# Kernel tuning notes

Measured on AMD Instinct MI355X. Metric: run time of the kernel, lower is better.

## Reference

```python
import jax, jax.numpy as jnp
import numpy as np

HEADS = 16
EMBED = 1024
HEAD_DIM = EMBED // HEADS


def setup_inputs() -> dict:
    key = jax.random.key(0)
    ks = jax.random.split(key, 10)
    B, SQ, SKV = 2, 2048, 2048
    s = 1.0 / np.sqrt(HEAD_DIM)
    sd = 1.0 / np.sqrt(EMBED)
    return {
        "queries": jax.random.normal(ks[0], (B, SQ, EMBED), jnp.float32),
        "values": jax.random.normal(ks[1], (B, SKV, EMBED), jnp.float32),
        "heads": HEADS,
        "Wv": jax.random.normal(ks[2], (HEAD_DIM, HEAD_DIM), jnp.float32) * s,
        "bv": jax.random.normal(ks[3], (HEAD_DIM,), jnp.float32) * 0.02,
        "Wk": jax.random.normal(ks[4], (HEAD_DIM, HEAD_DIM), jnp.float32) * s,
        "bk": jax.random.normal(ks[5], (HEAD_DIM,), jnp.float32) * 0.02,
        "Wq": jax.random.normal(ks[6], (HEAD_DIM, HEAD_DIM), jnp.float32) * s,
        "bq": jax.random.normal(ks[7], (HEAD_DIM,), jnp.float32) * 0.02,
        "Wd": jax.random.normal(ks[8], (EMBED, EMBED), jnp.float32) * sd,
        "bd": jax.random.normal(ks[9], (EMBED,), jnp.float32) * 0.02,
    }


def reference(queries, values, heads, Wv, bv, Wk, bk, Wq, bq, Wd, bd):
    n, sq, e = queries.shape
    skv = values.shape[1]
    d = e // heads
    # reshape to per-head layout [b, s, h, d]
    q_in = queries.reshape(n, sq, heads, d)
    v_in = values.reshape(n, skv, heads, d)
    # shared per-head linear projections (torch Linear: x @ W.T + b)
    v = jnp.einsum("bshd,ed->bshe", v_in, Wv) + bv
    # quirk preserved: keys computed from the ALREADY-PROJECTED values
    k = jnp.einsum("bshd,ed->bshe", v, Wk) + bk
    q = jnp.einsum("bshd,ed->bshe", q_in, Wq) + bq
    # full O(n^2) score matrix [b, h, sq, skv] (as in source)
    scores = jnp.einsum("bqhd,bkhd->bhqk", q, k) / jnp.sqrt(jnp.asarray(d, q.dtype))
    attn = jax.nn.softmax(scores, axis=-1)
    out = jnp.einsum("bhqk,bkhd->bqhd", attn, v).reshape(n, sq, e)
    return out @ Wd.T + bd
```

## Files before the change

kernel.cpp:

```cpp
#include <hip/hip_runtime.h>
#include <hip/hip_bf16.h>
#include <hip/hip_fp16.h>
#include <math.h>

typedef _Float16 f16;
typedef _Float16 f16x8 __attribute__((ext_vector_type(8)));
typedef _Float16 f16x4 __attribute__((ext_vector_type(4)));
typedef _Float16 f16x2 __attribute__((ext_vector_type(2)));
typedef unsigned short u16x8v __attribute__((ext_vector_type(8)));
typedef float f32x4 __attribute__((ext_vector_type(4)));

namespace {
constexpr int B = 2;
constexpr int H = 16;
constexpr int S = 2048;
constexpr int D = 64;
constexpr int E = 1024;
constexpr int LP = 72;
constexpr float QSCALE = 0.125f * 1.4426950408889634f;
}

#define GLOBAL_LOAD_LDS16(gp, lp)                                              \
  __builtin_amdgcn_global_load_lds(                                            \
      (const __attribute__((address_space(1))) void*)(gp),                     \
      (__attribute__((address_space(3))) void*)(lp), 16, 0, 0)

__global__ __launch_bounds__(256) void prep(const float* __restrict__ Wd, f16* __restrict__ wd16,
                                            const float* __restrict__ Wk, const float* __restrict__ Wv,
                                            const float* __restrict__ bv, const float* __restrict__ bk,
                                            float* __restrict__ Wkv, float* __restrict__ bkv) {
  if (blockIdx.x < 1024) {
    const int i = blockIdx.x * 256 + threadIdx.x;
    const float4 f = ((const float4*)Wd)[i];
    f16x4 o;
    o.x = (f16)f.x; o.y = (f16)f.y; o.z = (f16)f.z; o.w = (f16)f.w;
    *(f16x4*)(wd16 + 4 * (size_t)i) = o;
  } else {
    const int g = (blockIdx.x - 1024) * 256 + threadIdx.x;
    const int i = g >> 6, j = g & 63;
    float s = 0.f;
#pragma unroll 16
    for (int d = 0; d < 64; ++d) s = fmaf(Wk[i * 64 + d], Wv[d * 64 + j], s);
    Wkv[g] = s;
    if (g < 64) {
      float bb = bk[g];
#pragma unroll 16
      for (int d = 0; d < 64; ++d) bb = fmaf(Wk[g * 64 + d], bv[d], bb);
      bkv[g] = bb;
    }
  }
}

__global__ __launch_bounds__(256) void proj3_mfma(const float* __restrict__ xq,
                                                  const float* __restrict__ xv,
                                                  const float* __restrict__ Wq,
                                                  const float* __restrict__ bq,
                                                  const float* __restrict__ Wv,
                                                  const float* __restrict__ bv,
                                                  const float* __restrict__ Wkv,
                                                  const float* __restrict__ bkv,
                                                  f16* __restrict__ qp,
                                                  f16* __restrict__ vp,
                                                  f16* __restrict__ kp) {
  const int which = blockIdx.y;
  const float* x    = (which == 0) ? xq : xv;
  const float* W    = (which == 0) ? Wq : (which == 1) ? Wv : Wkv;
  const float* bias = (which == 0) ? bq : (which == 1) ? bv : bkv;
  f16* out          = (which == 0) ? qp : (which == 1) ? vp : kp;
  const float scale = (which == 0) ? QSCALE : 1.0f;

  const int t = threadIdx.x, lane = t & 63, w = t >> 6;
  const int l15 = lane & 15, quad = lane >> 4;
  const int m0 = (blockIdx.x * 4 + w) * 64;

  f16x8 wf[4][2], af[4][2];
#pragma unroll
  for (int nt = 0; nt < 4; ++nt)
#pragma unroll
    for (int kc = 0; kc < 2; ++kc) {
      const float* g = W + (size_t)(nt * 16 + l15) * 64 + kc * 32 + quad * 8;
      const float4 a = *(const float4*)g, b2 = *(const float4*)(g + 4);
      f16x8 v;
      v[0]=(f16)a.x; v[1]=(f16)a.y; v[2]=(f16)a.z; v[3]=(f16)a.w;
      v[4]=(f16)b2.x; v[5]=(f16)b2.y; v[6]=(f16)b2.z; v[7]=(f16)b2.w;
      wf[nt][kc] = v;
    }
#pragma unroll
  for (int mt = 0; mt < 4; ++mt)
#pragma unroll
    for (int kc = 0; kc < 2; ++kc) {
      const float* g = x + (size_t)(m0 + mt * 16 + l15) * 64 + kc * 32 + quad * 8;
      const float4 a = *(const float4*)g, b2 = *(const float4*)(g + 4);
      f16x8 v;
      v[0]=(f16)a.x; v[1]=(f16)a.y; v[2]=(f16)a.z; v[3]=(f16)a.w;
      v[4]=(f16)b2.x; v[5]=(f16)b2.y; v[6]=(f16)b2.z; v[7]=(f16)b2.w;
      af[mt][kc] = v;
    }

  f32x4 acc[4][4];
#pragma unroll
  for (int nt = 0; nt < 4; ++nt)
#pragma unroll
    for (int mt = 0; mt < 4; ++mt) acc[nt][mt] = (f32x4){0.f, 0.f, 0.f, 0.f};
#pragma unroll
  for (int kc = 0; kc < 2; ++kc)
#pragma unroll
    for (int nt = 0; nt < 4; ++nt)
#pragma unroll
      for (int mt = 0; mt < 4; ++mt)
        acc[nt][mt] = __builtin_amdgcn_mfma_f32_16x16x32_f16(wf[nt][kc], af[mt][kc], acc[nt][mt], 0, 0, 0);

  float4 bl4[4];
#pragma unroll
  for (int nt = 0; nt < 4; ++nt) bl4[nt] = *(const float4*)&bias[nt * 16 + quad * 4];

#pragma unroll
  for (int mt = 0; mt < 4; ++mt) {
    const int g = m0 + mt * 16 + l15;
    const int h = g & 15, bs_ = g >> 4;
    const int b = bs_ >> 11, s = bs_ & 2047;
    f16* o = out + ((size_t)(b * H + h) * S + s) * 64 + quad * 4;
#pragma unroll
    for (int nt = 0; nt < 4; ++nt) {
      const float p0 = (acc[nt][mt][0] + bl4[nt].x) * scale;
      const float p1 = (acc[nt][mt][1] + bl4[nt].y) * scale;
      const float p2 = (acc[nt][mt][2] + bl4[nt].z) * scale;
      const float p3 = (acc[nt][mt][3] + bl4[nt].w) * scale;
      union { f16x4 v4; f16x2 hh[2]; } u;
      u.hh[0] = __builtin_bit_cast(f16x2, __builtin_amdgcn_cvt_pkrtz(p0, p1));
      u.hh[1] = __builtin_bit_cast(f16x2, __builtin_amdgcn_cvt_pkrtz(p2, p3));
      *(f16x4*)(o + nt * 16) = u.v4;
    }
  }
}

__global__ __launch_bounds__(256) void attn_mfma(const f16* __restrict__ qp,
                                                 const f16* __restrict__ kp,
                                                 const f16* __restrict__ vp,
                                                 f16* __restrict__ ao) {
  __shared__ f16 ks[2][64 * LP];
  __shared__ f16 vt[2][64 * LP];
  __shared__ f16 ps[4 * 32 * LP];
  const int t = threadIdx.x, lane = t & 63, w = t >> 6;
  const int l15 = lane & 15, quad = lane >> 4;
  const int bh = blockIdx.x;
  const int q0 = blockIdx.y * 128;
  const f16* qbase = qp + ((size_t)bh * S + q0 + w * 32) * D;
  const f16* kbase = kp + (size_t)bh * S * D;
  const f16* vbase = vp + (size_t)bh * S * D;
  f16* pw = ps + w * 32 * LP;

  const int kr = t >> 2, kc0 = (t & 3) * 16;
  const int vd0 = (t >> 5) * 8, vpc0 = (t & 31) * 2;
  const int vkva = (vpc0 & 3) * 16 + (vpc0 >> 2);

  f16x8 qf[2][2];
#pragma unroll
  for (int mt = 0; mt < 2; ++mt)
#pragma unroll
    for (int kc = 0; kc < 2; ++kc)
      qf[mt][kc] = *(const f16x8*)(qbase + (size_t)(mt * 16 + l15) * D + kc * 32 + quad * 8);

  f16x8 vb4;
#pragma unroll
  for (int j = 0; j < 8; ++j) vb4[j] = (l15 == 0) ? (f16)1.0f : (f16)0.0f;

  f32x4 O[2][5];
#pragma unroll
  for (int mt = 0; mt < 2; ++mt)
#pragma unroll
    for (int nt = 0; nt < 5; ++nt) O[mt][nt] = (f32x4){0.f, 0.f, 0.f, 0.f};

  u16x8v ka, kb2, va, vb2;
  {
    const f16* gk = kbase + (size_t)kr * D + kc0;
    ka  = *(const u16x8v*)gk;
    kb2 = *(const u16x8v*)(gk + 8);
    const f16* gv = vbase + (size_t)vkva * D + vd0;
    va  = *(const u16x8v*)gv;
    vb2 = *(const u16x8v*)(gv + 16 * D);
  }
  {
    *(u16x8v*)&ks[0][kr * LP + kc0]     = ka;
    *(u16x8v*)&ks[0][kr * LP + kc0 + 8] = kb2;
#pragma unroll
    for (int j = 0; j < 8; ++j) {
      const unsigned pk = (unsigned)va[j] | ((unsigned)vb2[j] << 16);
      *(unsigned*)&vt[0][(vd0 + j) * LP + vpc0] = pk;
    }
  }

  int cur = 0;
  for (int kt = 0; kt < S / 64; ++kt) {
    if (kt + 1 < S / 64) {
      const f16* gk = kbase + ((size_t)(kt + 1) * 64 + kr) * D + kc0;
      ka  = *(const u16x8v*)gk;
      kb2 = *(const u16x8v*)(gk + 8);
      const f16* gv = vbase + ((size_t)(kt + 1) * 64 + vkva) * D + vd0;
      va  = *(const u16x8v*)gv;
      vb2 = *(const u16x8v*)(gv + 16 * D);
    }
    __asm__ volatile("s_waitcnt lgkmcnt(0)" ::: "memory");
    __builtin_amdgcn_s_barrier();
    __asm__ volatile("" ::: "memory");

    f32x4 sc[2][4];
#pragma unroll
    for (int mt = 0; mt < 2; ++mt)
#pragma unroll
      for (int nt = 0; nt < 4; ++nt) sc[mt][nt] = (f32x4){0.f, 0.f, 0.f, 0.f};
    __builtin_amdgcn_s_setprio(1);
#pragma unroll
    for (int kc = 0; kc < 2; ++kc)
#pragma unroll
      for (int nt = 0; nt < 4; ++nt) {
        const f16x8 bf = *(const f16x8*)&ks[cur][(nt * 16 + l15) * LP + kc * 32 + quad * 8];
#pragma unroll
        for (int mt = 0; mt < 2; ++mt)
          sc[mt][nt] = __builtin_amdgcn_mfma_f32_16x16x32_f16(qf[mt][kc], bf, sc[mt][nt], 0, 0, 0);
      }
    __builtin_amdgcn_s_setprio(0);

#pragma unroll
    for (int mt = 0; mt < 2; ++mt)
#pragma unroll
      for (int r = 0; r < 4; ++r) {
        const float p0 = __builtin_amdgcn_exp2f(sc[mt][0][r]);
        const float p1 = __builtin_amdgcn_exp2f(sc[mt][1][r]);
        const float p2 = __builtin_amdgcn_exp2f(sc[mt][2][r]);
        const float p3 = __builtin_amdgcn_exp2f(sc[mt][3][r]);
        union { f16x4 v4; f16x2 h[2]; } u;
        u.h[0] = __builtin_bit_cast(f16x2, __builtin_amdgcn_cvt_pkrtz(p0, p1));
        u.h[1] = __builtin_bit_cast(f16x2, __builtin_amdgcn_cvt_pkrtz(p2, p3));
        *(f16x4*)&pw[(mt * 16 + quad * 4 + r) * LP + l15 * 4] = u.v4;
      }
    __asm__ volatile("s_waitcnt lgkmcnt(0)" ::: "memory");

    f16x8 pa[2][2];
#pragma unroll
    for (int mt = 0; mt < 2; ++mt)
#pragma unroll
      for (int kc = 0; kc < 2; ++kc)
        pa[mt][kc] = *(const f16x8*)&pw[(mt * 16 + l15) * LP + kc * 32 + quad * 8];
    __builtin_amdgcn_s_setprio(1);
#pragma unroll
    for (int kc = 0; kc < 2; ++kc) {
#pragma unroll
      for (int nt = 0; nt < 4; ++nt) {
        const f16x8 vbf = *(const f16x8*)&vt[cur][(nt * 16 + l15) * LP + kc * 32 + quad * 8];
#pragma unroll
        for (int mt = 0; mt < 2; ++mt)
          O[mt][nt] = __builtin_amdgcn_mfma_f32_16x16x32_f16(pa[mt][kc], vbf, O[mt][nt], 0, 0, 0);
      }
#pragma unroll
      for (int mt = 0; mt < 2; ++mt)
        O[mt][4] = __builtin_amdgcn_mfma_f32_16x16x32_f16(pa[mt][kc], vb4, O[mt][4], 0, 0, 0);
    }
    __builtin_amdgcn_s_setprio(0);

    if (kt + 1 < S / 64) {
      const int nb = cur ^ 1;
      *(u16x8v*)&ks[nb][kr * LP + kc0]     = ka;
      *(u16x8v*)&ks[nb][kr * LP + kc0 + 8] = kb2;
#pragma unroll
      for (int j = 0; j < 8; ++j) {
        const unsigned pk = (unsigned)va[j] | ((unsigned)vb2[j] << 16);
        *(unsigned*)&vt[nb][(vd0 + j) * LP + vpc0] = pk;
      }
    }
    cur ^= 1;
  }

  const int b = bh >> 4, h = bh & 15;
#pragma unroll
  for (int mt = 0; mt < 2; ++mt)
#pragma unroll
    for (int r = 0; r < 4; ++r) {
      const float l = __shfl(O[mt][4][r], quad << 4, 64);
      const float inv = 1.f / l;
      const int row = q0 + w * 32 + mt * 16 + quad * 4 + r;
      f16* o = ao + ((size_t)b * S + row) * E + h * D;
#pragma unroll
      for (int nt = 0; nt < 4; ++nt)
        o[nt * 16 + l15] = (f16)(O[mt][nt][r] * inv);
    }
}

__global__ __launch_bounds__(256) void dense_mfma(const f16* __restrict__ A,
                                                  const f16* __restrict__ Wd16,
                                                  const float* __restrict__ bd,
                                                  float* __restrict__ out) {
  __shared__ f16 as[2][128 * 64];
  __shared__ f16 bs[2][128 * 64];
  const int t = threadIdx.x;
  const int lane = t & 63;
  const int w = t >> 6;
  const int l15 = lane & 15;
  const int quad = lane >> 4;
  const int m0 = blockIdx.x * 128;
  const int n0 = blockIdx.y * 128;
  const int wm = (w >> 1) * 64, wn = (w & 1) * 64;

  const int srow = (lane >> 3);
  const int scol = (lane & 7) * 8;
  const f16* ga0 = A    + (size_t)(m0 + w * 32 + srow) * E + scol;
  const f16* gb0 = Wd16 + (size_t)(n0 + w * 32 + srow) * E + scol;

  constexpr int NT = E / 64;

  f32x4 acc[4][4];
#pragma unroll
  for (int mt = 0; mt < 4; ++mt)
#pragma unroll
    for (int nt = 0; nt < 4; ++nt) acc[mt][nt] = (f32x4){0.f, 0.f, 0.f, 0.f};

#pragma unroll
  for (int i = 0; i < 4; ++i) {
    GLOBAL_LOAD_LDS16(ga0 + (size_t)(i * 8) * E, &as[0][(w * 32 + i * 8) * 64]);
    GLOBAL_LOAD_LDS16(gb0 + (size_t)(i * 8) * E, &bs[0][(w * 32 + i * 8) * 64]);
  }
  __syncthreads();

  int cur = 0;
  for (int kt = 0; kt < NT; ++kt) {
    if (kt + 1 < NT) {
      const int nb = cur ^ 1;
#pragma unroll
      for (int i = 0; i < 4; ++i) {
        GLOBAL_LOAD_LDS16(ga0 + (size_t)(i * 8) * E + (kt + 1) * 64, &as[nb][(w * 32 + i * 8) * 64]);
        GLOBAL_LOAD_LDS16(gb0 + (size_t)(i * 8) * E + (kt + 1) * 64, &bs[nb][(w * 32 + i * 8) * 64]);
      }
    }
    f16x8 af[4][2];
#pragma unroll
    for (int mt = 0; mt < 4; ++mt)
#pragma unroll
      for (int kc = 0; kc < 2; ++kc)
        af[mt][kc] = *(const f16x8*)&as[cur][(wm + mt * 16 + l15) * 64 + kc * 32 + quad * 8];
#pragma unroll
    for (int kc = 0; kc < 2; ++kc)
#pragma unroll
      for (int nt = 0; nt < 4; ++nt) {
        const f16x8 bf = *(const f16x8*)&bs[cur][(wn + nt * 16 + l15) * 64 + kc * 32 + quad * 8];
#pragma unroll
        for (int mt = 0; mt < 4; ++mt)
          acc[mt][nt] = __builtin_amdgcn_mfma_f32_16x16x32_f16(af[mt][kc], bf, acc[mt][nt], 0, 0, 0);
      }
    __syncthreads();
    cur ^= 1;
  }

#pragma unroll
  for (int nt = 0; nt < 4; ++nt) {
    const int col = n0 + wn + nt * 16 + l15;
    const float bdv = bd[col];
#pragma unroll
    for (int mt = 0; mt < 4; ++mt)
#pragma unroll
      for (int r = 0; r < 4; ++r)
        out[(size_t)(m0 + wm + mt * 16 + quad * 4 + r) * E + col] = acc[mt][nt][r] + bdv;
  }
}

extern "C" void kernel_launch(void* const* d_in, const int* in_sizes, int n_in,
                              void* d_out, int out_size, void* d_ws, size_t ws_size,
                              hipStream_t stream) {
  const float* queries = (const float*)d_in[0];
  const float* values  = (const float*)d_in[1];
  const float* Wv = (const float*)d_in[3];
  const float* bv = (const float*)d_in[4];
  const float* Wk = (const float*)d_in[5];
  const float* bk = (const float*)d_in[6];
  const float* Wq = (const float*)d_in[7];
  const float* bq = (const float*)d_in[8];
  const float* Wd = (const float*)d_in[9];
  const float* bd = (const float*)d_in[10];
  float* out = (float*)d_out;

  char* ws = (char*)d_ws;
  f16* qp    = (f16*)(ws);
  f16* kp    = (f16*)(ws + 8u * 1024 * 1024);
  f16* vp    = (f16*)(ws + 16u * 1024 * 1024);
  f16* ao    = (f16*)(ws + 24u * 1024 * 1024);
  f16* wd16  = (f16*)(ws + 32u * 1024 * 1024);
  float* wkv = (float*)(ws + 34u * 1024 * 1024);
  float* bkv = (float*)(ws + 34u * 1024 * 1024 + 16384);
  (void)ws_size; (void)in_sizes; (void)n_in; (void)out_size;

  prep<<<1040, 256, 0, stream>>>(Wd, wd16, Wk, Wv, bv, bk, wkv, bkv);
  proj3_mfma<<<dim3(256, 3), 256, 0, stream>>>(queries, values, Wq, bq, Wv, bv, wkv, bkv, qp, vp, kp);
  attn_mfma<<<dim3(B * H, S / 128), 256, 0, stream>>>(qp, kp, vp, ao);
  dense_mfma<<<dim3(B * S / 128, E / 128), 256, 0, stream>>>(ao, wd16, bd, out);
}
```

Measured before the change: 187.9 us.

## Swizzle LDS tiles, keep P in registers, and share values load across projections

```diff
diff --git a/kernel.cpp b/kernel.cpp
--- a/kernel.cpp
+++ b/kernel.cpp
@@ -16,7 +16,6 @@
 constexpr int S = 2048;
 constexpr int D = 64;
 constexpr int E = 1024;
-constexpr int LP = 72;
 constexpr float QSCALE = 0.125f * 1.4426950408889634f;
 }
 
@@ -63,28 +62,13 @@
                                                   f16* __restrict__ vp,
                                                   f16* __restrict__ kp) {
   const int which = blockIdx.y;
-  const float* x    = (which == 0) ? xq : xv;
-  const float* W    = (which == 0) ? Wq : (which == 1) ? Wv : Wkv;
-  const float* bias = (which == 0) ? bq : (which == 1) ? bv : bkv;
-  f16* out          = (which == 0) ? qp : (which == 1) ? vp : kp;
-  const float scale = (which == 0) ? QSCALE : 1.0f;
+  const float* x = which ? xv : xq;
 
   const int t = threadIdx.x, lane = t & 63, w = t >> 6;
   const int l15 = lane & 15, quad = lane >> 4;
   const int m0 = (blockIdx.x * 4 + w) * 64;
 
-  f16x8 wf[4][2], af[4][2];
-#pragma unroll
-  for (int nt = 0; nt < 4; ++nt)
-#pragma unroll
-    for (int kc = 0; kc < 2; ++kc) {
-      const float* g = W + (size_t)(nt * 16 + l15) * 64 + kc * 32 + quad * 8;
-      const float4 a = *(const float4*)g, b2 = *(const float4*)(g + 4);
-      f16x8 v;
-      v[0]=(f16)a.x; v[1]=(f16)a.y; v[2]=(f16)a.z; v[3]=(f16)a.w;
-      v[4]=(f16)b2.x; v[5]=(f16)b2.y; v[6]=(f16)b2.z; v[7]=(f16)b2.w;
-      wf[nt][kc] = v;
-    }
+  f16x8 af[4][2];
 #pragma unroll
   for (int mt = 0; mt < 4; ++mt)
 #pragma unroll
@@ -97,39 +81,60 @@
       af[mt][kc] = v;
     }
 
-  f32x4 acc[4][4];
-#pragma unroll
-  for (int nt = 0; nt < 4; ++nt)
-#pragma unroll
-    for (int mt = 0; mt < 4; ++mt) acc[nt][mt] = (f32x4){0.f, 0.f, 0.f, 0.f};
-#pragma unroll
-  for (int kc = 0; kc < 2; ++kc)
+  const int npass = which ? 2 : 1;
+  for (int pass = 0; pass < npass; ++pass) {
+    const float* W    = which ? (pass ? Wkv : Wv) : Wq;
+    const float* bias = which ? (pass ? bkv : bv) : bq;
+    f16* out          = which ? (pass ? kp : vp) : qp;
+    const float scale = which ? 1.0f : QSCALE;
+
+    f16x8 wf[4][2];
 #pragma unroll
     for (int nt = 0; nt < 4; ++nt)
 #pragma unroll
-      for (int mt = 0; mt < 4; ++mt)
-        acc[nt][mt] = __builtin_amdgcn_mfma_f32_16x16x32_f16(wf[nt][kc], af[mt][kc], acc[nt][mt], 0, 0, 0);
-
-  float4 bl4[4];
-#pragma unroll
-  for (int nt = 0; nt < 4; ++nt) bl4[nt] = *(const float4*)&bias[nt * 16 + quad * 4];
-
-#pragma unroll
-  for (int mt = 0; mt < 4; ++mt) {
-    const int g = m0 + mt * 16 + l15;
-    const int h = g & 15, bs_ = g >> 4;
-    const int b = bs_ >> 11, s = bs_ & 2047;
-    f16* o = out + ((size_t)(b * H + h) * S + s) * 64 + quad * 4;
-#pragma unroll
-    for (int nt = 0; nt < 4; ++nt) {
-      const float p0 = (acc[nt][mt][0] + bl4[nt].x) * scale;
-      const float p1 = (acc[nt][mt][1] + bl4[nt].y) * scale;
-      const float p2 = (acc[nt][mt][2] + bl4[nt].z) * scale;
-      const float p3 = (acc[nt][mt][3] + bl4[nt].w) * scale;
-      union { f16x4 v4; f16x2 hh[2]; } u;
-      u.hh[0] = __builtin_bit_cast(f16x2, __builtin_amdgcn_cvt_pkrtz(p0, p1));
-      u.hh[1] = __builtin_bit_cast(f16x2, __builtin_amdgcn_cvt_pkrtz(p2, p3));
-      *(f16x4*)(o + nt * 16) = u.v4;
+      for (int kc = 0; kc < 2; ++kc) {
+        const float* g = W + (size_t)(nt * 16 + l15) * 64 + kc * 32 + quad * 8;
+        const float4 a = *(const float4*)g, b2 = *(const float4*)(g + 4);
+        f16x8 v;
+        v[0]=(f16)a.x; v[1]=(f16)a.y; v[2]=(f16)a.z; v[3]=(f16)a.w;
+        v[4]=(f16)b2.x; v[5]=(f16)b2.y; v[6]=(f16)b2.z; v[7]=(f16)b2.w;
+        wf[nt][kc] = v;
+      }
+
+    f32x4 acc[4][4];
+#pragma unroll
+    for (int nt = 0; nt < 4; ++nt)
+#pragma unroll
+      for (int mt = 0; mt < 4; ++mt) acc[nt][mt] = (f32x4){0.f, 0.f, 0.f, 0.f};
+#pragma unroll
+    for (int kc = 0; kc < 2; ++kc)
+#pragma unroll
+      for (int nt = 0; nt < 4; ++nt)
+#pragma unroll
+        for (int mt = 0; mt < 4; ++mt)
+          acc[nt][mt] = __builtin_amdgcn_mfma_f32_16x16x32_f16(wf[nt][kc], af[mt][kc], acc[nt][mt], 0, 0, 0);
+
+    float4 bl4[4];
+#pragma unroll
+    for (int nt = 0; nt < 4; ++nt) bl4[nt] = *(const float4*)&bias[nt * 16 + quad * 4];
+
+#pragma unroll
+    for (int mt = 0; mt < 4; ++mt) {
+      const int g = m0 + mt * 16 + l15;
+      const int h = g & 15, bs_ = g >> 4;
+      const int b = bs_ >> 11, s = bs_ & 2047;
+      f16* o = out + ((size_t)(b * H + h) * S + s) * 64 + quad * 4;
+#pragma unroll
+      for (int nt = 0; nt < 4; ++nt) {
+        const float p0 = (acc[nt][mt][0] + bl4[nt].x) * scale;
+        const float p1 = (acc[nt][mt][1] + bl4[nt].y) * scale;
+        const float p2 = (acc[nt][mt][2] + bl4[nt].z) * scale;
+        const float p3 = (acc[nt][mt][3] + bl4[nt].w) * scale;
+        union { f16x4 v4; f16x2 hh[2]; } u;
+        u.hh[0] = __builtin_bit_cast(f16x2, __builtin_amdgcn_cvt_pkrtz(p0, p1));
+        u.hh[1] = __builtin_bit_cast(f16x2, __builtin_amdgcn_cvt_pkrtz(p2, p3));
+        *(f16x4*)(o + nt * 16) = u.v4;
+      }
     }
   }
 }
@@ -138,9 +143,8 @@
                                                  const f16* __restrict__ kp,
                                                  const f16* __restrict__ vp,
                                                  f16* __restrict__ ao) {
-  __shared__ f16 ks[2][64 * LP];
-  __shared__ f16 vt[2][64 * LP];
-  __shared__ f16 ps[4 * 32 * LP];
+  __shared__ f16 ks[2][64 * 64];
+  __shared__ f16 vt[2][64 * 64];
   const int t = threadIdx.x, lane = t & 63, w = t >> 6;
   const int l15 = lane & 15, quad = lane >> 4;
   const int bh = blockIdx.x;
@@ -148,11 +152,12 @@
   const f16* qbase = qp + ((size_t)bh * S + q0 + w * 32) * D;
   const f16* kbase = kp + (size_t)bh * S * D;
   const f16* vbase = vp + (size_t)bh * S * D;
-  f16* pw = ps + w * 32 * LP;
-
-  const int kr = t >> 2, kc0 = (t & 3) * 16;
-  const int vd0 = (t >> 5) * 8, vpc0 = (t & 31) * 2;
-  const int vkva = (vpc0 & 3) * 16 + (vpc0 >> 2);
+
+  const int kr = t >> 2, kc2 = (t & 3) * 2;
+  const int vd0 = (t >> 5) * 8;
+  const int p0 = (t & 31) * 2;
+  const int vkv = ((p0 >> 5) << 5) | (((p0 & 7) >> 2) << 4) | (((p0 >> 3) & 3) << 2) | (p0 & 3);
+  const int vchunk = p0 >> 3, vsub = p0 & 7;
 
   f16x8 qf[2][2];
 #pragma unroll
@@ -173,81 +178,79 @@
 
   u16x8v ka, kb2, va, vb2;
   {
-    const f16* gk = kbase + (size_t)kr * D + kc0;
+    const f16* gk = kbase + (size_t)kr * D + kc2 * 8;
     ka  = *(const u16x8v*)gk;
     kb2 = *(const u16x8v*)(gk + 8);
-    const f16* gv = vbase + (size_t)vkva * D + vd0;
+    const f16* gv = vbase + (size_t)vkv * D + vd0;
     va  = *(const u16x8v*)gv;
-    vb2 = *(const u16x8v*)(gv + 16 * D);
+    vb2 = *(const u16x8v*)(gv + D);
   }
   {
-    *(u16x8v*)&ks[0][kr * LP + kc0]     = ka;
-    *(u16x8v*)&ks[0][kr * LP + kc0 + 8] = kb2;
+    *(u16x8v*)&ks[0][kr * 64 + ((kc2 ^ (kr & 7)) * 8)]       = ka;
+    *(u16x8v*)&ks[0][kr * 64 + (((kc2 + 1) ^ (kr & 7)) * 8)] = kb2;
 #pragma unroll
     for (int j = 0; j < 8; ++j) {
+      const int d = vd0 + j;
       const unsigned pk = (unsigned)va[j] | ((unsigned)vb2[j] << 16);
-      *(unsigned*)&vt[0][(vd0 + j) * LP + vpc0] = pk;
+      *(unsigned*)&vt[0][d * 64 + ((vchunk ^ (d & 7)) * 8) + vsub] = pk;
     }
   }
 
   int cur = 0;
   for (int kt = 0; kt < S / 64; ++kt) {
     if (kt + 1 < S / 64) {
-      const f16* gk = kbase + ((size_t)(kt + 1) * 64 + kr) * D + kc0;
+      const f16* gk = kbase + ((size_t)(kt + 1) * 64 + kr) * D + kc2 * 8;
       ka  = *(const u16x8v*)gk;
       kb2 = *(const u16x8v*)(gk + 8);
-      const f16* gv = vbase + ((size_t)(kt + 1) * 64 + vkva) * D + vd0;
+      const f16* gv = vbase + ((size_t)(kt + 1) * 64 + vkv) * D + vd0;
       va  = *(const u16x8v*)gv;
-      vb2 = *(const u16x8v*)(gv + 16 * D);
+      vb2 = *(const u16x8v*)(gv + D);
     }
     __asm__ volatile("s_waitcnt lgkmcnt(0)" ::: "memory");
     __builtin_amdgcn_s_barrier();
     __asm__ volatile("" ::: "memory");
 
-    f32x4 sc[2][4];
+    f32x4 sc[4][2];
+#pragma unroll
+    for (int nt = 0; nt < 4; ++nt)
+#pragma unroll
+      for (int mt = 0; mt < 2; ++mt) sc[nt][mt] = (f32x4){0.f, 0.f, 0.f, 0.f};
+    __builtin_amdgcn_s_setprio(1);
+#pragma unroll
+    for (int kc = 0; kc < 2; ++kc)
+#pragma unroll
+      for (int nt = 0; nt < 4; ++nt) {
+        const f16x8 kf = *(const f16x8*)&ks[cur][(nt * 16 + l15) * 64 + (((kc * 4 + quad) ^ (l15 & 7)) * 8)];
+#pragma unroll
+        for (int mt = 0; mt < 2; ++mt)
+          sc[nt][mt] = __builtin_amdgcn_mfma_f32_16x16x32_f16(kf, qf[mt][kc], sc[nt][mt], 0, 0, 0);
+      }
+    __builtin_amdgcn_s_setprio(0);
+
+    f16x8 pa[2][2];
 #pragma unroll
     for (int mt = 0; mt < 2; ++mt)
 #pragma unroll
-      for (int nt = 0; nt < 4; ++nt) sc[mt][nt] = (f32x4){0.f, 0.f, 0.f, 0.f};
+      for (int kc = 0; kc < 2; ++kc) {
+        const f32x4 s0 = sc[2 * kc][mt], s1 = sc[2 * kc + 1][mt];
+        union { f16x8 v8; f16x2 h[4]; } u;
+        u.h[0] = __builtin_bit_cast(f16x2, __builtin_amdgcn_cvt_pkrtz(
+            __builtin_amdgcn_exp2f(s0[0]), __builtin_amdgcn_exp2f(s0[1])));
+        u.h[1] = __builtin_bit_cast(f16x2, __builtin_amdgcn_cvt_pkrtz(
+            __builtin_amdgcn_exp2f(s0[2]), __builtin_amdgcn_exp2f(s0[3])));
+        u.h[2] = __builtin_bit_cast(f16x2, __builtin_amdgcn_cvt_pkrtz(
+            __builtin_amdgcn_exp2f(s1[0]), __builtin_amdgcn_exp2f(s1[1])));
+        u.h[3] = __builtin_bit_cast(f16x2, __builtin_amdgcn_cvt_pkrtz(
+            __builtin_amdgcn_exp2f(s1[2]), __builtin_amdgcn_exp2f(s1[3])));
+        pa[mt][kc] = u.v8;
+      }
+
     __builtin_amdgcn_s_setprio(1);
 #pragma unroll
-    for (int kc = 0; kc < 2; ++kc)
+    for (int kc = 0; kc < 2; ++kc) {
 #pragma unroll
       for (int nt = 0; nt < 4; ++nt) {
-        const f16x8 bf = *(const f16x8*)&ks[cur][(nt * 16 + l15) * LP + kc * 32 + quad * 8];
-#pragma unroll
-        for (int mt = 0; mt < 2; ++mt)
-          sc[mt][nt] = __builtin_amdgcn_mfma_f32_16x16x32_f16(qf[mt][kc], bf, sc[mt][nt], 0, 0, 0);
-      }
-    __builtin_amdgcn_s_setprio(0);
-
-#pragma unroll
-    for (int mt = 0; mt < 2; ++mt)
-#pragma unroll
-      for (int r = 0; r < 4; ++r) {
-        const float p0 = __builtin_amdgcn_exp2f(sc[mt][0][r]);
-        const float p1 = __builtin_amdgcn_exp2f(sc[mt][1][r]);
-        const float p2 = __builtin_amdgcn_exp2f(sc[mt][2][r]);
-        const float p3 = __builtin_amdgcn_exp2f(sc[mt][3][r]);
-        union { f16x4 v4; f16x2 h[2]; } u;
-        u.h[0] = __builtin_bit_cast(f16x2, __builtin_amdgcn_cvt_pkrtz(p0, p1));
-        u.h[1] = __builtin_bit_cast(f16x2, __builtin_amdgcn_cvt_pkrtz(p2, p3));
-        *(f16x4*)&pw[(mt * 16 + quad * 4 + r) * LP + l15 * 4] = u.v4;
-      }
-    __asm__ volatile("s_waitcnt lgkmcnt(0)" ::: "memory");
-
-    f16x8 pa[2][2];
-#pragma unroll
-    for (int mt = 0; mt < 2; ++mt)
-#pragma unroll
-      for (int kc = 0; kc < 2; ++kc)
-        pa[mt][kc] = *(const f16x8*)&pw[(mt * 16 + l15) * LP + kc * 32 + quad * 8];
-    __builtin_amdgcn_s_setprio(1);
-#pragma unroll
-    for (int kc = 0; kc < 2; ++kc) {
-#pragma unroll
-      for (int nt = 0; nt < 4; ++nt) {
-        const f16x8 vbf = *(const f16x8*)&vt[cur][(nt * 16 + l15) * LP + kc * 32 + quad * 8];
+        const f16x8 vbf = *(const f16x8*)&vt[cur][(nt * 16 + l15) * 64 + (((kc * 4 + quad) ^ (l15 & 7)) * 8)];
 #pragma unroll
         for (int mt = 0; mt < 2; ++mt)
           O[mt][nt] = __builtin_amdgcn_mfma_f32_16x16x32_f16(pa[mt][kc], vbf, O[mt][nt], 0, 0, 0);
@@ -260,12 +263,13 @@
 
     if (kt + 1 < S / 64) {
       const int nb = cur ^ 1;
-      *(u16x8v*)&ks[nb][kr * LP + kc0]     = ka;
-      *(u16x8v*)&ks[nb][kr * LP + kc0 + 8] = kb2;
+      *(u16x8v*)&ks[nb][kr * 64 + ((kc2 ^ (kr & 7)) * 8)]       = ka;
+      *(u16x8v*)&ks[nb][kr * 64 + (((kc2 + 1) ^ (kr & 7)) * 8)] = kb2;
 #pragma unroll
       for (int j = 0; j < 8; ++j) {
+        const int d = vd0 + j;
         const unsigned pk = (unsigned)va[j] | ((unsigned)vb2[j] << 16);
-        *(unsigned*)&vt[nb][(vd0 + j) * LP + vpc0] = pk;
+        *(unsigned*)&vt[nb][d * 64 + ((vchunk ^ (d & 7)) * 8) + vsub] = pk;
       }
     }
     cur ^= 1;
@@ -302,9 +306,9 @@
   const int wm = (w >> 1) * 64, wn = (w & 1) * 64;
 
   const int srow = (lane >> 3);
-  const int scol = (lane & 7) * 8;
-  const f16* ga0 = A    + (size_t)(m0 + w * 32 + srow) * E + scol;
-  const f16* gb0 = Wd16 + (size_t)(n0 + w * 32 + srow) * E + scol;
+  const int schunk = (lane & 7) ^ srow;
+  const f16* ga0 = A    + (size_t)(m0 + w * 32 + srow) * E + schunk * 8;
+  const f16* gb0 = Wd16 + (size_t)(n0 + w * 32 + srow) * E + schunk * 8;
 
   constexpr int NT = E / 64;
 
@@ -336,12 +340,12 @@
     for (int mt = 0; mt < 4; ++mt)
 #pragma unroll
       for (int kc = 0; kc < 2; ++kc)
-        af[mt][kc] = *(const f16x8*)&as[cur][(wm + mt * 16 + l15) * 64 + kc * 32 + quad * 8];
+        af[mt][kc] = *(const f16x8*)&as[cur][(wm + mt * 16 + l15) * 64 + (((kc * 4 + quad) ^ (l15 & 7)) * 8)];
 #pragma unroll
     for (int kc = 0; kc < 2; ++kc)
 #pragma unroll
       for (int nt = 0; nt < 4; ++nt) {
-        const f16x8 bf = *(const f16x8*)&bs[cur][(wn + nt * 16 + l15) * 64 + kc * 32 + quad * 8];
+        const f16x8 bf = *(const f16x8*)&bs[cur][(wn + nt * 16 + l15) * 64 + (((kc * 4 + quad) ^ (l15 & 7)) * 8)];
 #pragma unroll
         for (int mt = 0; mt < 4; ++mt)
           acc[mt][nt] = __builtin_amdgcn_mfma_f32_16x16x32_f16(af[mt][kc], bf, acc[mt][nt], 0, 0, 0);
@@ -388,7 +392,7 @@
   (void)ws_size; (void)in_sizes; (void)n_in; (void)out_size;
 
   prep<<<1040, 256, 0, stream>>>(Wd, wd16, Wk, Wv, bv, bk, wkv, bkv);
-  proj3_mfma<<<dim3(256, 3), 256, 0, stream>>>(queries, values, Wq, bq, Wv, bv, wkv, bkv, qp, vp, kp);
+  proj3_mfma<<<dim3(256, 2), 256, 0, stream>>>(queries, values, Wq, bq, Wv, bv, wkv, bkv, qp, vp, kp);
   attn_mfma<<<dim3(B * H, S / 128), 256, 0, stream>>>(qp, kp, vp, ao);
   dense_mfma<<<dim3(B * S / 128, E / 128), 256, 0, stream>>>(ao, wd16, bd, out);
 }
```

Measured after the change: 186.1 us. About the same (-0.9%).
